# Optimization experiments

Hardware: AMD Instinct MI355X
Metric: run time of the kernel (lower is better)

The kernel has to match this reference:

```python
import jax, jax.numpy as jnp
import numpy as np

B, L, D, H = 8, 1024, 512, 8
EPS = 1e-5

def setup_inputs() -> dict:
    key = jax.random.key(0)
    ks = jax.random.split(key, 12)
    s = lambda fan_in: 1.0 / np.sqrt(fan_in)
    u = lambda k, shape, sc: jax.random.uniform(k, shape, jnp.float32, -sc, sc)
    return {
        "input": jax.random.normal(ks[0], (B, L, D), jnp.float32),
        "wq": u(ks[1], (D, H * D), s(D)), "bq": u(ks[2], (H * D,), s(D)),
        "wk": u(ks[3], (D, H * D), s(D)), "bk": u(ks[4], (H * D,), s(D)),
        "wv": u(ks[5], (D, H * D), s(D)), "bv": u(ks[6], (H * D,), s(D)),
        "score_w": u(ks[7], (2 * D, 1), s(2 * D)), "score_b": u(ks[8], (1,), s(2 * D)),
        "fc_w": u(ks[9], (H * D, D), s(H * D)), "fc_b": u(ks[10], (D,), s(H * D)),
        "ln_g": jnp.ones((D,), jnp.float32), "ln_b": jnp.zeros((D,), jnp.float32),
    }

def reference(input, wq, bq, wk, bk, wv, bv, score_w, score_b, fc_w, fc_b, ln_g, ln_b):
    x = input
    b, l, d = x.shape
    h = wq.shape[1] // d
    # project and fold heads into leading batch dim: (h*b, l, d)
    def proj(w, bias):
        y = (x @ w + bias).reshape(b, l, h, d)
        return y.transpose(2, 0, 1, 3).reshape(h * b, l, d)
    q = proj(wq, bq)
    k = proj(wk, bk)
    v = proj(wv, bv)
    # _score(cat(k_i, q_j)) decomposed: k part uses score_w[:d], q part score_w[d:]
    sk = (k @ score_w[:d])[:, :, 0]   # (h*b, l) -> row index i
    sq = (q @ score_w[d:])[:, :, 0]   # (h*b, l) -> col index j
    kq = jnp.tanh(sk[:, :, None] + sq[:, None, :] + score_b[0])  # (h*b, l, l)
    # faithful to original bug: softmax over trailing size-1 dim -> all ones
    score = jax.nn.softmax(kq[..., None], axis=-1)[..., 0]       # (h*b, l, l)
    out = jnp.einsum('nij,njd->nid', score, v)                   # (h*b, l, d)
    out = out.reshape(h, b, l, d).transpose(1, 2, 0, 3).reshape(b, l, h * d)
    out = out @ fc_w + fc_b
    y = out + x
    mu = jnp.mean(y, axis=-1, keepdims=True)
    var = jnp.var(y, axis=-1, keepdims=True)
    return (y - mu) / jnp.sqrt(var + EPS) * ln_g + ln_b
```

## Files before the change

kernel.cpp:

```cpp
#include <hip/hip_runtime.h>

#define BB 8
#define LL 1024
#define DD 512
#define HDIM 4096
#define EPS_LN 1e-5f
#define NB 512
#define NT 512
#define POISON_I ((int)0xAAAAAAAAu)
#define ARRIVALS 64


__device__ __forceinline__ void batch_bar(int* cnt) {
    asm volatile("s_waitcnt vmcnt(0)" ::: "memory");
    __syncthreads();
    if (threadIdx.x == 0) {
        __hip_atomic_fetch_add(cnt, 1, __ATOMIC_RELAXED,
                               __HIP_MEMORY_SCOPE_AGENT);
        while (__hip_atomic_load(cnt, __ATOMIC_RELAXED,
                                 __HIP_MEMORY_SCOPE_AGENT) !=
               POISON_I + ARRIVALS)
            __builtin_amdgcn_s_sleep(1);
        asm volatile("" ::: "memory");
    }
    __syncthreads();
}

__global__ __launch_bounds__(NT, 4) void mha_fused(
    const float* __restrict__ x,
    const float* __restrict__ wv,
    const float* __restrict__ bv,
    const float* __restrict__ fcw,
    const float* __restrict__ fcb,
    const float* __restrict__ g,
    const float* __restrict__ beta,
    float* __restrict__ out,
    float* __restrict__ xs,
    float* __restrict__ u,
    int* __restrict__ bar)
{
    __shared__ float redA[8][DD];
    __shared__ float xs_b[DD];
    __shared__ float Tpart[8][64];
    __shared__ float T_l[64];
    __shared__ float uf[DD];

    const int tid = threadIdx.x;
    const int bi  = blockIdx.x;
    const int b   = bi >> 6;
    const int j   = bi & 63;

    const int dv   = tid & 63;
    const int rowg = tid >> 6;
    const int cI = dv;
    const int kg = rowg;

    float4 xa0, xa1, xb0, xb1;
    float  wpre[48];

    const float* wcol = wv + (size_t)(j * 64) + cI;
    {
        const float* basep = x + ((size_t)(bi * 16 + rowg * 2)) * DD + dv * 8;
        xa0 = *(const float4*)(basep);
        xa1 = *(const float4*)(basep + 4);
        xb0 = *(const float4*)(basep + DD);
        xb1 = *(const float4*)(basep + DD + 4);

#pragma unroll
        for (int i = 0; i < 48; ++i)
            wpre[i] = wcol[(size_t)(kg * 64 + i) * HDIM];

        float4* dst = (float4*)&redA[rowg][dv * 8];
        dst[0] = make_float4(xa0.x + xb0.x, xa0.y + xb0.y,
                             xa0.z + xb0.z, xa0.w + xb0.w);
        dst[1] = make_float4(xa1.x + xb1.x, xa1.y + xb1.y,
                             xa1.z + xb1.z, xa1.w + xb1.w);
        __syncthreads();

        float s = 0.f;
#pragma unroll
        for (int gg = 0; gg < 8; ++gg) s += redA[gg][tid];
        atomicAdd(&xs[b * DD + tid], s);
    }

    batch_bar(bar + b * 32);

    {
        xs_b[tid] = xs[b * DD + tid];
        __syncthreads();

        float t = 0.f;
#pragma unroll
        for (int i = 0; i < 48; ++i)
            t += xs_b[kg * 64 + i] * wpre[i];
#pragma unroll
        for (int i = 48; i < 64; ++i)
            t += xs_b[kg * 64 + i] * wcol[(size_t)(kg * 64 + i) * HDIM];
        Tpart[kg][cI] = t;
        __syncthreads();

        if (tid < 64) {
            float s = 0.f;
#pragma unroll
            for (int q = 0; q < 8; ++q) s += Tpart[q][tid];
            T_l[tid] = s + 1024.f * bv[j * 64 + tid];
        }
        __syncthreads();

        float a = 0.f;
        const float* frow = fcw + (size_t)(j * 64) * DD + tid;
#pragma unroll 8
        for (int c = 0; c < 64; ++c)
            a += T_l[c] * frow[(size_t)c * DD];
        atomicAdd(&u[b * DD + tid], a);
    }

    float4 g0  = *(const float4*)(g + dv * 8);
    float4 g1  = *(const float4*)(g + dv * 8 + 4);
    float4 bt0 = *(const float4*)(beta + dv * 8);
    float4 bt1 = *(const float4*)(beta + dv * 8 + 4);
    float  fpre = fcb[tid];

    batch_bar(bar + (8 + b) * 32);

    {
        uf[tid] = u[b * DD + tid] + fpre;
        __syncthreads();

        float4 uq0 = *(const float4*)(uf + dv * 8);
        float4 uq1 = *(const float4*)(uf + dv * 8 + 4);

#pragma unroll
        for (int it = 0; it < 2; ++it) {
            const int row = bi * 16 + rowg * 2 + it;
            const size_t off = (size_t)row * DD + dv * 8;
            float4 x0 = (it == 0) ? xa0 : xb0;
            float4 x1 = (it == 0) ? xa1 : xb1;

            float y[8];
            y[0] = x0.x + uq0.x;  y[1] = x0.y + uq0.y;
            y[2] = x0.z + uq0.z;  y[3] = x0.w + uq0.w;
            y[4] = x1.x + uq1.x;  y[5] = x1.y + uq1.y;
            y[6] = x1.z + uq1.z;  y[7] = x1.w + uq1.w;

            float s1 = 0.f, ss = 0.f;
#pragma unroll
            for (int i = 0; i < 8; ++i) { s1 += y[i]; ss += y[i] * y[i]; }
#pragma unroll
            for (int m = 1; m < 64; m <<= 1) {
                s1 += __shfl_xor(s1, m, 64);
                ss += __shfl_xor(ss, m, 64);
            }
            const float mean = s1 * (1.f / 512.f);
            const float var  = ss * (1.f / 512.f) - mean * mean;
            const float rstd = rsqrtf(var + EPS_LN);

            float4 o0, o1;
            o0.x = (y[0] - mean) * rstd * g0.x + bt0.x;
            o0.y = (y[1] - mean) * rstd * g0.y + bt0.y;
            o0.z = (y[2] - mean) * rstd * g0.z + bt0.z;
            o0.w = (y[3] - mean) * rstd * g0.w + bt0.w;
            o1.x = (y[4] - mean) * rstd * g1.x + bt1.x;
            o1.y = (y[5] - mean) * rstd * g1.y + bt1.y;
            o1.z = (y[6] - mean) * rstd * g1.z + bt1.z;
            o1.w = (y[7] - mean) * rstd * g1.w + bt1.w;
            *(float4*)(out + off)     = o0;
            *(float4*)(out + off + 4) = o1;
        }
    }
}

extern "C" void kernel_launch(void* const* d_in, const int* in_sizes, int n_in,
                              void* d_out, int out_size, void* d_ws, size_t ws_size,
                              hipStream_t stream) {
    const float* x   = (const float*)d_in[0];
    const float* wv  = (const float*)d_in[5];
    const float* bv  = (const float*)d_in[6];
    const float* fcw = (const float*)d_in[9];
    const float* fcb = (const float*)d_in[10];
    const float* lng = (const float*)d_in[11];
    const float* lnb = (const float*)d_in[12];

    float* xs  = (float*)d_ws;
    int*   bar = (int*)((char*)d_ws + 16 * 1024);
    float* u   = (float*)((char*)d_ws + 32 * 1024);
    float* out = (float*)d_out;

    mha_fused<<<NB, NT, 0, stream>>>(x, wv, bv, fcw, fcb, lng, lnb,
                                     out, xs, u, bar);
}
```

Measured before the change: 140.2 us.

## Double block size to 1024 threads and drop register weight prefetch

Raises threads per block from 512 to 1024 so each wave handles one input row instead of two. The Wv column dot product is split over 16 groups of 32 instead of 8 groups of 64, and the fc step is split into two 32-row halves. The 48-register prefetch of Wv before the first grid barrier is removed, so those weights are now loaded after the barrier. The aim is more memory-level parallelism and lower register pressure, but the weight loads are no longer hidden behind the barrier wait and atomic traffic into u doubles.

```diff
diff --git a/kernel.cpp b/kernel.cpp
--- a/kernel.cpp
+++ b/kernel.cpp
@@ -6,7 +6,7 @@
 #define HDIM 4096
 #define EPS_LN 1e-5f
 #define NB 512
-#define NT 512
+#define NT 1024
 #define POISON_I ((int)0xAAAAAAAAu)
 #define ARRIVALS 64
 
@@ -26,7 +26,7 @@
     __syncthreads();
 }
 
-__global__ __launch_bounds__(NT, 4) void mha_fused(
+__global__ __launch_bounds__(NT, 8) void mha_fused(
     const float* __restrict__ x,
     const float* __restrict__ wv,
     const float* __restrict__ bv,
@@ -39,9 +39,9 @@
     float* __restrict__ u,
     int* __restrict__ bar)
 {
-    __shared__ float redA[8][DD];
+    __shared__ float redA[16][DD];
     __shared__ float xs_b[DD];
-    __shared__ float Tpart[8][64];
+    __shared__ float Tpart[16][64];
     __shared__ float T_l[64];
     __shared__ float uf[DD];
 
@@ -50,123 +50,111 @@
     const int b   = bi >> 6;
     const int j   = bi & 63;
 
-    const int dv   = tid & 63;
-    const int rowg = tid >> 6;
-    const int cI = dv;
-    const int kg = rowg;
+    const int dv  = tid & 63;
+    const int wid = tid >> 6;
 
-    float4 xa0, xa1, xb0, xb1;
-    float  wpre[48];
+    float4 xr0, xr1;
 
-    const float* wcol = wv + (size_t)(j * 64) + cI;
     {
-        const float* basep = x + ((size_t)(bi * 16 + rowg * 2)) * DD + dv * 8;
-        xa0 = *(const float4*)(basep);
-        xa1 = *(const float4*)(basep + 4);
-        xb0 = *(const float4*)(basep + DD);
-        xb1 = *(const float4*)(basep + DD + 4);
+        const float* basep = x + ((size_t)(bi * 16 + wid)) * DD + dv * 8;
+        xr0 = *(const float4*)(basep);
+        xr1 = *(const float4*)(basep + 4);
 
-#pragma unroll
-        for (int i = 0; i < 48; ++i)
-            wpre[i] = wcol[(size_t)(kg * 64 + i) * HDIM];
-
-        float4* dst = (float4*)&redA[rowg][dv * 8];
-        dst[0] = make_float4(xa0.x + xb0.x, xa0.y + xb0.y,
-                             xa0.z + xb0.z, xa0.w + xb0.w);
-        dst[1] = make_float4(xa1.x + xb1.x, xa1.y + xb1.y,
-                             xa1.z + xb1.z, xa1.w + xb1.w);
+        float4* dst = (float4*)&redA[wid][dv * 8];
+        dst[0] = xr0;
+        dst[1] = xr1;
         __syncthreads();
 
-        float s = 0.f;
+        if (tid < DD) {
+            float s = 0.f;
 #pragma unroll
-        for (int gg = 0; gg < 8; ++gg) s += redA[gg][tid];
-        atomicAdd(&xs[b * DD + tid], s);
+            for (int gg = 0; gg < 16; ++gg) s += redA[gg][tid];
+            atomicAdd(&xs[b * DD + tid], s);
+        }
     }
 
     batch_bar(bar + b * 32);
 
     {
-        xs_b[tid] = xs[b * DD + tid];
+        if (tid < DD) xs_b[tid] = xs[b * DD + tid];
         __syncthreads();
 
+        const int cI = dv;
+        const int kg = wid;
         float t = 0.f;
-#pragma unroll
-        for (int i = 0; i < 48; ++i)
-            t += xs_b[kg * 64 + i] * wpre[i];
-#pragma unroll
-        for (int i = 48; i < 64; ++i)
-            t += xs_b[kg * 64 + i] * wcol[(size_t)(kg * 64 + i) * HDIM];
+        const float* wcol = wv + (size_t)(j * 64) + cI;
+#pragma unroll 8
+        for (int i = 0; i < 32; ++i) {
+            const int k = kg * 32 + i;
+            t += xs_b[k] * wcol[(size_t)k * HDIM];
+        }
         Tpart[kg][cI] = t;
         __syncthreads();
 
         if (tid < 64) {
             float s = 0.f;
 #pragma unroll
-            for (int q = 0; q < 8; ++q) s += Tpart[q][tid];
+            for (int q = 0; q < 16; ++q) s += Tpart[q][tid];
             T_l[tid] = s + 1024.f * bv[j * 64 + tid];
         }
         __syncthreads();
 
+        const int dd = tid & 511;
+        const int ch = tid >> 9;
         float a = 0.f;
-        const float* frow = fcw + (size_t)(j * 64) * DD + tid;
+        const float* frow = fcw + (size_t)(j * 64 + ch * 32) * DD + dd;
 #pragma unroll 8
-        for (int c = 0; c < 64; ++c)
-            a += T_l[c] * frow[(size_t)c * DD];
-        atomicAdd(&u[b * DD + tid], a);
+        for (int i = 0; i < 32; ++i)
+            a += T_l[ch * 32 + i] * frow[(size_t)i * DD];
+        atomicAdd(&u[b * DD + dd], a);
     }
-
-    float4 g0  = *(const float4*)(g + dv * 8);
-    float4 g1  = *(const float4*)(g + dv * 8 + 4);
-    float4 bt0 = *(const float4*)(beta + dv * 8);
-    float4 bt1 = *(const float4*)(beta + dv * 8 + 4);
-    float  fpre = fcb[tid];
 
     batch_bar(bar + (8 + b) * 32);
 
     {
-        uf[tid] = u[b * DD + tid] + fpre;
+        if (tid < DD) uf[tid] = u[b * DD + tid] + fcb[tid];
         __syncthreads();
 
         float4 uq0 = *(const float4*)(uf + dv * 8);
         float4 uq1 = *(const float4*)(uf + dv * 8 + 4);
 
+        const int row = bi * 16 + wid;
+        const size_t off = (size_t)row * DD + dv * 8;
+
+        float y[8];
+        y[0] = xr0.x + uq0.x;  y[1] = xr0.y + uq0.y;
+        y[2] = xr0.z + uq0.z;  y[3] = xr0.w + uq0.w;
+        y[4] = xr1.x + uq1.x;  y[5] = xr1.y + uq1.y;
+        y[6] = xr1.z + uq1.z;  y[7] = xr1.w + uq1.w;
+
+        float s1 = 0.f, ss = 0.f;
 #pragma unroll
-        for (int it = 0; it < 2; ++it) {
-            const int row = bi * 16 + rowg * 2 + it;
-            const size_t off = (size_t)row * DD + dv * 8;
-            float4 x0 = (it == 0) ? xa0 : xb0;
-            float4 x1 = (it == 0) ? xa1 : xb1;
+        for (int i = 0; i < 8; ++i) { s1 += y[i]; ss += y[i] * y[i]; }
+#pragma unroll
+        for (int m = 1; m < 64; m <<= 1) {
+            s1 += __shfl_xor(s1, m, 64);
+            ss += __shfl_xor(ss, m, 64);
+        }
+        const float mean = s1 * (1.f / 512.f);
+        const float var  = ss * (1.f / 512.f) - mean * mean;
+        const float rstd = rsqrtf(var + EPS_LN);
 
-            float y[8];
-            y[0] = x0.x + uq0.x;  y[1] = x0.y + uq0.y;
-            y[2] = x0.z + uq0.z;  y[3] = x0.w + uq0.w;
-            y[4] = x1.x + uq1.x;  y[5] = x1.y + uq1.y;
-            y[6] = x1.z + uq1.z;  y[7] = x1.w + uq1.w;
+        float4 g0  = *(const float4*)(g + dv * 8);
+        float4 g1  = *(const float4*)(g + dv * 8 + 4);
+        float4 bt0 = *(const float4*)(beta + dv * 8);
+        float4 bt1 = *(const float4*)(beta + dv * 8 + 4);
 
-            float s1 = 0.f, ss = 0.f;
-#pragma unroll
-            for (int i = 0; i < 8; ++i) { s1 += y[i]; ss += y[i] * y[i]; }
-#pragma unroll
-            for (int m = 1; m < 64; m <<= 1) {
-                s1 += __shfl_xor(s1, m, 64);
-                ss += __shfl_xor(ss, m, 64);
-            }
-            const float mean = s1 * (1.f / 512.f);
-            const float var  = ss * (1.f / 512.f) - mean * mean;
-            const float rstd = rsqrtf(var + EPS_LN);
-
-            float4 o0, o1;
-            o0.x = (y[0] - mean) * rstd * g0.x + bt0.x;
-            o0.y = (y[1] - mean) * rstd * g0.y + bt0.y;
-            o0.z = (y[2] - mean) * rstd * g0.z + bt0.z;
-            o0.w = (y[3] - mean) * rstd * g0.w + bt0.w;
-            o1.x = (y[4] - mean) * rstd * g1.x + bt1.x;
-            o1.y = (y[5] - mean) * rstd * g1.y + bt1.y;
-            o1.z = (y[6] - mean) * rstd * g1.z + bt1.z;
-            o1.w = (y[7] - mean) * rstd * g1.w + bt1.w;
-            *(float4*)(out + off)     = o0;
-            *(float4*)(out + off + 4) = o1;
-        }
+        float4 o0, o1;
+        o0.x = (y[0] - mean) * rstd * g0.x + bt0.x;
+        o0.y = (y[1] - mean) * rstd * g0.y + bt0.y;
+        o0.z = (y[2] - mean) * rstd * g0.z + bt0.z;
+        o0.w = (y[3] - mean) * rstd * g0.w + bt0.w;
+        o1.x = (y[4] - mean) * rstd * g1.x + bt1.x;
+        o1.y = (y[5] - mean) * rstd * g1.y + bt1.y;
+        o1.z = (y[6] - mean) * rstd * g1.z + bt1.z;
+        o1.w = (y[7] - mean) * rstd * g1.w + bt1.w;
+        *(float4*)(out + off)     = o0;
+        *(float4*)(out + off + 4) = o1;
     }
 }
 
```

Result: faster. 127.7 us (-9.0%).

## Split fused kernel into producer and consumer block roles with global counters

Applied to the files above, without the earlier changes.

Replaces the uniform 512-block kernel, which used per-batch barriers, with 256 blocks of 1024 threads in two roles. 128 weight blocks stage slices of wv and fc_w into shared memory and compute the projected vector u for all 8 batches at once. 128 row blocks compute the per-batch column sums, signal a global counter, wait for u, then re-read x and apply the residual and layernorm. The aim is to overlap weight loading with the x reduction and to stop re-reading weights per batch. In exchange it relies on all blocks being co-resident for the spin waits, uses large shared memory per block, and reads x twice.

```diff
diff --git a/kernel.cpp b/kernel.cpp
--- a/kernel.cpp
+++ b/kernel.cpp
@@ -5,28 +5,13 @@
 #define DD 512
 #define HDIM 4096
 #define EPS_LN 1e-5f
-#define NB 512
-#define NT 512
+#define NBLK 256
+#define NT 1024
+#define NW 128
 #define POISON_I ((int)0xAAAAAAAAu)
-#define ARRIVALS 64
-
-
-__device__ __forceinline__ void batch_bar(int* cnt) {
-    asm volatile("s_waitcnt vmcnt(0)" ::: "memory");
-    __syncthreads();
-    if (threadIdx.x == 0) {
-        __hip_atomic_fetch_add(cnt, 1, __ATOMIC_RELAXED,
-                               __HIP_MEMORY_SCOPE_AGENT);
-        while (__hip_atomic_load(cnt, __ATOMIC_RELAXED,
-                                 __HIP_MEMORY_SCOPE_AGENT) !=
-               POISON_I + ARRIVALS)
-            __builtin_amdgcn_s_sleep(1);
-        asm volatile("" ::: "memory");
-    }
-    __syncthreads();
-}
-
-__global__ __launch_bounds__(NT, 4) void mha_fused(
+
+
+__global__ __launch_bounds__(NT) void mha_roles(
     const float* __restrict__ x,
     const float* __restrict__ wv,
     const float* __restrict__ bv,
@@ -39,103 +24,159 @@
     float* __restrict__ u,
     int* __restrict__ bar)
 {
-    __shared__ float redA[8][DD];
-    __shared__ float xs_b[DD];
-    __shared__ float Tpart[8][64];
-    __shared__ float T_l[64];
-    __shared__ float uf[DD];
-
-    const int tid = threadIdx.x;
-    const int bi  = blockIdx.x;
-    const int b   = bi >> 6;
-    const int j   = bi & 63;
-
-    const int dv   = tid & 63;
-    const int rowg = tid >> 6;
-    const int cI = dv;
-    const int kg = rowg;
-
-    float4 xa0, xa1, xb0, xb1;
-    float  wpre[48];
-
-    const float* wcol = wv + (size_t)(j * 64) + cI;
-    {
-        const float* basep = x + ((size_t)(bi * 16 + rowg * 2)) * DD + dv * 8;
-        xa0 = *(const float4*)(basep);
-        xa1 = *(const float4*)(basep + 4);
-        xb0 = *(const float4*)(basep + DD);
-        xb1 = *(const float4*)(basep + DD + 4);
-
-#pragma unroll
-        for (int i = 0; i < 48; ++i)
-            wpre[i] = wcol[(size_t)(kg * 64 + i) * HDIM];
-
-        float4* dst = (float4*)&redA[rowg][dv * 8];
-        dst[0] = make_float4(xa0.x + xb0.x, xa0.y + xb0.y,
-                             xa0.z + xb0.z, xa0.w + xb0.w);
-        dst[1] = make_float4(xa1.x + xb1.x, xa1.y + xb1.y,
-                             xa1.z + xb1.z, xa1.w + xb1.w);
-        __syncthreads();
-
-        float s = 0.f;
-#pragma unroll
-        for (int gg = 0; gg < 8; ++gg) s += redA[gg][tid];
-        atomicAdd(&xs[b * DD + tid], s);
-    }
-
-    batch_bar(bar + b * 32);
-
-    {
-        xs_b[tid] = xs[b * DD + tid];
-        __syncthreads();
-
+    __shared__ float smem[33056];
+
+    const int tid  = threadIdx.x;
+    const int bi   = blockIdx.x;
+    const int lane = tid & 63;
+    const int wid  = tid >> 6;
+
+    int* xs_cnt = bar;
+    int* u_cnt  = bar + 64;
+
+    if (bi < NW) {
+        const int j  = bi;
+        const int c0 = j * 32;
+        float* wv_s  = smem;
+        float* fcw_s = smem + 16384;
+        float* T_s   = smem + 32768;
+        float* bv_s  = smem + 33024;
+
+        float4 wb[4], fb[4];
+#pragma unroll
+        for (int i = 0; i < 4; ++i) {
+            const int f = tid + i * 1024;
+            const int k = f >> 3, cg = f & 7;
+            wb[i] = *(const float4*)(wv + (size_t)k * HDIM + c0 + cg * 4);
+        }
+#pragma unroll
+        for (int i = 0; i < 4; ++i) {
+            const int f = tid + i * 1024;
+            fb[i] = *(const float4*)(fcw + (size_t)c0 * DD + (size_t)f * 4);
+        }
+#pragma unroll
+        for (int i = 0; i < 4; ++i)
+            *(float4*)(wv_s + (size_t)(tid + i * 1024) * 4) = wb[i];
+#pragma unroll
+        for (int i = 0; i < 4; ++i)
+            *(float4*)(fcw_s + (size_t)(tid + i * 1024) * 4) = fb[i];
+        if (tid < 32) bv_s[tid] = bv[c0 + tid];
+
+        if (tid == 0) {
+            while (__hip_atomic_load(xs_cnt, __ATOMIC_RELAXED,
+                                     __HIP_MEMORY_SCOPE_AGENT) !=
+                   POISON_I + 128)
+                __builtin_amdgcn_s_sleep(1);
+            asm volatile("" ::: "memory");
+        }
+        __syncthreads();
+
+        const int p = tid >> 2;
+        const int q = tid & 3;
+        const int b = p >> 5, c = p & 31;
+        const float* xrow = xs + b * DD + q * 128;
         float t = 0.f;
-#pragma unroll
-        for (int i = 0; i < 48; ++i)
-            t += xs_b[kg * 64 + i] * wpre[i];
-#pragma unroll
-        for (int i = 48; i < 64; ++i)
-            t += xs_b[kg * 64 + i] * wcol[(size_t)(kg * 64 + i) * HDIM];
-        Tpart[kg][cI] = t;
-        __syncthreads();
-
-        if (tid < 64) {
-            float s = 0.f;
-#pragma unroll
-            for (int q = 0; q < 8; ++q) s += Tpart[q][tid];
-            T_l[tid] = s + 1024.f * bv[j * 64 + tid];
-        }
-        __syncthreads();
-
-        float a = 0.f;
-        const float* frow = fcw + (size_t)(j * 64) * DD + tid;
 #pragma unroll 8
-        for (int c = 0; c < 64; ++c)
-            a += T_l[c] * frow[(size_t)c * DD];
-        atomicAdd(&u[b * DD + tid], a);
-    }
-
-    float4 g0  = *(const float4*)(g + dv * 8);
-    float4 g1  = *(const float4*)(g + dv * 8 + 4);
-    float4 bt0 = *(const float4*)(beta + dv * 8);
-    float4 bt1 = *(const float4*)(beta + dv * 8 + 4);
-    float  fpre = fcb[tid];
-
-    batch_bar(bar + (8 + b) * 32);
-
-    {
-        uf[tid] = u[b * DD + tid] + fpre;
-        __syncthreads();
-
-        float4 uq0 = *(const float4*)(uf + dv * 8);
-        float4 uq1 = *(const float4*)(uf + dv * 8 + 4);
-
-#pragma unroll
-        for (int it = 0; it < 2; ++it) {
-            const int row = bi * 16 + rowg * 2 + it;
-            const size_t off = (size_t)row * DD + dv * 8;
-            float4 x0 = (it == 0) ? xa0 : xb0;
-            float4 x1 = (it == 0) ? xa1 : xb1;
+        for (int i = 0; i < 128; ++i)
+            t += xrow[i] * wv_s[(q * 128 + i) * 32 + c];
+        t += __shfl_xor(t, 1, 64);
+        t += __shfl_xor(t, 2, 64);
+        if (q == 0) T_s[p] = t + 1024.f * bv_s[c];
+        __syncthreads();
+
+        const int d = tid & 511;
+        const int h = tid >> 9;
+        float acc[8] = {0.f, 0.f, 0.f, 0.f, 0.f, 0.f, 0.f, 0.f};
+#pragma unroll
+        for (int cc = 0; cc < 16; ++cc) {
+            const int lc = h * 16 + cc;
+            const float fw = fcw_s[lc * 512 + d];
+#pragma unroll
+            for (int b2 = 0; b2 < 8; ++b2)
+                acc[b2] += T_s[b2 * 32 + lc] * fw;
+        }
+        float* ured = smem;
+        if (h == 1) {
+#pragma unroll
+            for (int b2 = 0; b2 < 8; ++b2) ured[b2 * 512 + d] = acc[b2];
+        }
+        __syncthreads();
+        if (h == 0) {
+#pragma unroll
+            for (int b2 = 0; b2 < 8; ++b2)
+                atomicAdd(&u[b2 * DD + d], acc[b2] + ured[b2 * 512 + d]);
+        }
+
+        asm volatile("s_waitcnt vmcnt(0)" ::: "memory");
+        __syncthreads();
+        if (tid == 0)
+            __hip_atomic_fetch_add(u_cnt, 1, __ATOMIC_RELAXED,
+                                   __HIP_MEMORY_SCOPE_AGENT);
+    } else {
+        const int xb = bi - NW;
+        const int b  = xb >> 4;
+        const int s  = xb & 15;
+        const int r0 = b * 1024 + s * 64;
+        float* redA = smem;
+        float* uf   = smem + 4096;
+
+        float va[8] = {0.f, 0.f, 0.f, 0.f, 0.f, 0.f, 0.f, 0.f};
+        const float* rbase = x + (size_t)(r0 + wid) * DD + lane * 8;
+#pragma unroll
+        for (int it = 0; it < 4; ++it) {
+            float4 p0 = *(const float4*)(rbase + (size_t)it * 16 * DD);
+            float4 p1 = *(const float4*)(rbase + (size_t)it * 16 * DD + 4);
+            va[0] += p0.x; va[1] += p0.y; va[2] += p0.z; va[3] += p0.w;
+            va[4] += p1.x; va[5] += p1.y; va[6] += p1.z; va[7] += p1.w;
+        }
+        if (wid < 8) {
+#pragma unroll
+            for (int i = 0; i < 8; ++i) redA[wid * 512 + lane * 8 + i] = va[i];
+        }
+        __syncthreads();
+        if (wid >= 8) {
+#pragma unroll
+            for (int i = 0; i < 8; ++i)
+                redA[(wid - 8) * 512 + lane * 8 + i] += va[i];
+        }
+        __syncthreads();
+        if (tid < 512) {
+            float ssum = 0.f;
+#pragma unroll
+            for (int gg = 0; gg < 8; ++gg) ssum += redA[gg * 512 + tid];
+            atomicAdd(&xs[b * DD + tid], ssum);
+        }
+
+        asm volatile("s_waitcnt vmcnt(0)" ::: "memory");
+        __syncthreads();
+        if (tid == 0)
+            __hip_atomic_fetch_add(xs_cnt, 1, __ATOMIC_RELAXED,
+                                   __HIP_MEMORY_SCOPE_AGENT);
+
+        float4 g0  = *(const float4*)(g + lane * 8);
+        float4 g1  = *(const float4*)(g + lane * 8 + 4);
+        float4 bt0 = *(const float4*)(beta + lane * 8);
+        float4 bt1 = *(const float4*)(beta + lane * 8 + 4);
+
+        if (tid == 0) {
+            while (__hip_atomic_load(u_cnt, __ATOMIC_RELAXED,
+                                     __HIP_MEMORY_SCOPE_AGENT) !=
+                   POISON_I + 128)
+                __builtin_amdgcn_s_sleep(1);
+            asm volatile("" ::: "memory");
+        }
+        __syncthreads();
+
+        if (tid < 512) uf[tid] = u[b * DD + tid] + fcb[tid];
+        __syncthreads();
+
+        float4 uq0 = *(const float4*)(uf + lane * 8);
+        float4 uq1 = *(const float4*)(uf + lane * 8 + 4);
+#pragma unroll
+        for (int it = 0; it < 4; ++it) {
+            const size_t off = (size_t)(r0 + wid + it * 16) * DD + lane * 8;
+            float4 x0 = *(const float4*)(x + off);
+            float4 x1 = *(const float4*)(x + off + 4);
 
             float y[8];
             y[0] = x0.x + uq0.x;  y[1] = x0.y + uq0.y;
@@ -186,6 +227,6 @@
     float* u   = (float*)((char*)d_ws + 32 * 1024);
     float* out = (float*)d_out;
 
-    mha_fused<<<NB, NT, 0, stream>>>(x, wv, bv, fcw, fcb, lng, lnb,
-                                     out, xs, u, bar);
+    mha_roles<<<NBLK, NT, 0, stream>>>(x, wv, bv, fcw, fcb, lng, lnb,
+                                       out, xs, u, bar);
 }
```

Measured after the change: 137.8 us. No clear change (-1.7%).
